# Optimization experiments

Hardware: AMD Instinct MI355X
Metric: run time of the kernel (lower is better)

Reference implementation:

```python
import jax, jax.numpy as jnp
import numpy as np

NUM_NODES = 25
EMBED_DIM = 64
OUT_SIZE = 2
N_TOTAL = 204800   # 8192 graphs * 25 nodes
N_EDGES = 3276800  # avg degree 16


def setup_inputs() -> dict:
    key = jax.random.key(0)
    ks = jax.random.split(key, 8)
    x = jax.random.normal(ks[0], (N_TOTAL, EMBED_DIM), dtype=jnp.float32)
    # random edges; real graphs are graph-local but math is identical
    edge_index = jax.random.randint(ks[1], (2, N_EDGES), 0, N_TOTAL, dtype=jnp.int32)
    batch = jnp.repeat(jnp.arange(N_TOTAL // NUM_NODES, dtype=jnp.int32), NUM_NODES)
    hid = NUM_NODES * EMBED_DIM  # 1600
    W_conv = jax.random.normal(ks[2], (EMBED_DIM, EMBED_DIM), dtype=jnp.float32) / np.sqrt(EMBED_DIM)
    b_conv = jnp.zeros((EMBED_DIM,), dtype=jnp.float32)
    W1 = jax.random.normal(ks[3], (hid, hid), dtype=jnp.float32) / np.sqrt(hid)
    b1 = jnp.zeros((hid,), dtype=jnp.float32)
    W2 = jax.random.normal(ks[4], (hid, OUT_SIZE), dtype=jnp.float32) / np.sqrt(hid)
    b2 = jnp.zeros((OUT_SIZE,), dtype=jnp.float32)
    return {"x": x, "edge_index": edge_index, "batch": batch,
            "W_conv": W_conv, "b_conv": b_conv,
            "W1": W1, "b1": b1, "W2": W2, "b2": b2}


def reference(x, edge_index, batch, W_conv, b_conv, W1, b1, W2, b2):
    N = x.shape[0]
    # --- GCNConv: add self-loops, symmetric degree norm, transform, scatter-add ---
    loop = jnp.arange(N, dtype=edge_index.dtype)
    src = jnp.concatenate([edge_index[0], loop])
    dst = jnp.concatenate([edge_index[1], loop])
    deg = jax.ops.segment_sum(jnp.ones_like(dst, dtype=x.dtype), dst, num_segments=N)
    dinv = jax.lax.rsqrt(deg)  # deg >= 1 due to self-loops
    norm = dinv[src] * dinv[dst]                       # [E+N]
    h = x @ W_conv                                     # [N, D]
    msg = h[src] * norm[:, None]                       # gather + scale
    h = jax.ops.segment_sum(msg, dst, num_segments=N) + b_conv
    h = jax.nn.relu(h)
    # --- dense head ---
    nb = -(-batch.shape[0] // NUM_NODES)               # ceil
    h = h.reshape(nb, NUM_NODES * EMBED_DIM)           # [B, 1600]
    h = jax.nn.relu(h @ W1 + b1)
    logits = h @ W2 + b2
    return jax.nn.softmax(logits, axis=-1)
```

## Files before the change

kernel.cpp:

```cpp
#include <hip/hip_runtime.h>
#include <hip/hip_bf16.h>
#include <stdint.h>

#define NT   204800
#define NE   3276800
#define ED   64
#define NBG  8192
#define HID  1600
#define HPAD 1664
#define CAP  56
#define NBKT 400
#define BCAP 9216

typedef float  f32x4  __attribute__((ext_vector_type(4)));
typedef __bf16 bf16x8 __attribute__((ext_vector_type(8)));

__device__ __forceinline__ void async_ld16(const void* g, void* l) {
    __builtin_amdgcn_global_load_lds(
        (__attribute__((address_space(1))) const void*)g,
        (__attribute__((address_space(3))) void*)l, 16, 0, 0);
}

__device__ __forceinline__ unsigned short f2bf_raw(float f) {
    __hip_bfloat16 h = __float2bfloat16(f);
    return *(unsigned short*)&h;
}

__global__ void k_initg(int* __restrict__ gcur) {
    int t = threadIdx.x;
    if (t < NBKT) gcur[t] = t * BCAP;
}

__global__ __launch_bounds__(256) void k_part(const int* __restrict__ srcv,
                                              const int* __restrict__ dstv,
                                              int* __restrict__ gcur,
                                              unsigned* __restrict__ rec) {
    __shared__ int hist[NBKT];
    __shared__ int slot[NBKT];
    __shared__ int gofs[NBKT];
    const int t = threadIdx.x;
    const int base = blockIdx.x * (NE / 512);
    for (int i = t; i < NBKT; i += 256) { hist[i] = 0; slot[i] = 0; }
    __syncthreads();
    for (int j = 0; j < 25; ++j) {
        int d = dstv[base + j * 256 + t];
        atomicAdd(&hist[d >> 9], 1);
    }
    __syncthreads();
    for (int i = t; i < NBKT; i += 256) gofs[i] = atomicAdd(&gcur[i], hist[i]);
    __syncthreads();
    for (int j = 0; j < 25; ++j) {
        int i = base + j * 256 + t;
        int d = dstv[i];
        int s = srcv[i];
        int b = d >> 9;
        int ls = atomicAdd(&slot[b], 1);
        int idx = gofs[b] + ls;
        if (idx < (b + 1) * BCAP)
            rec[idx] = ((unsigned)s << 9) | (unsigned)(d & 511);
    }
}

__global__ __launch_bounds__(512) void k_fillb(const int* __restrict__ gcur,
                                               const unsigned* __restrict__ rec,
                                               int* __restrict__ cur,
                                               int* __restrict__ csr,
                                               float* __restrict__ dinv) {
    __shared__ int cnt[512];
    const int t = threadIdx.x;
    const int b = blockIdx.x;
    const int n0 = b * 512;
    cnt[t] = 0;
    __syncthreads();
    const int bstart = b * BCAP;
    int bcnt = gcur[b] - bstart;
    bcnt = (bcnt > BCAP) ? BCAP : bcnt;
    for (int idx = t; idx < bcnt; idx += 512) {
        unsigned r = rec[bstart + idx];
        unsigned rel = r & 511u;
        int ls = atomicAdd(&cnt[rel], 1);
        if (ls < CAP) csr[(size_t)(n0 + rel) * CAP + ls] = (int)(r >> 9);
    }
    __syncthreads();
    int cn = cnt[t];
    cur[n0 + t] = cn;
    dinv[n0 + t] = rsqrtf((float)cn + 1.f);
}

__global__ __launch_bounds__(256) void k_gemm_conv(const float* __restrict__ x,
                                                   const float* __restrict__ Wc,
                                                   const float* __restrict__ dinv,
                                                   __hip_bfloat16* __restrict__ hbs) {
    __shared__ unsigned short Xs[64 * 72];
    __shared__ unsigned short Wt[64 * 72];
    const int t = threadIdx.x;
    const int row0 = blockIdx.x * 64;
#pragma unroll
    for (int i = 0; i < 4; ++i) {
        int idx = i * 256 + t;
        int r = idx >> 4, c4 = (idx & 15) << 2;
        f32x4 wv = ((const f32x4*)Wc)[idx];
        Wt[(c4 + 0) * 72 + r] = f2bf_raw(wv.x);
        Wt[(c4 + 1) * 72 + r] = f2bf_raw(wv.y);
        Wt[(c4 + 2) * 72 + r] = f2bf_raw(wv.z);
        Wt[(c4 + 3) * 72 + r] = f2bf_raw(wv.w);
        f32x4 xv = ((const f32x4*)(x + (size_t)row0 * 64))[idx];
        ushort4 p;
        p.x = f2bf_raw(xv.x);
        p.y = f2bf_raw(xv.y);
        p.z = f2bf_raw(xv.z);
        p.w = f2bf_raw(xv.w);
        *(ushort4*)&Xs[r * 72 + c4] = p;
    }
    __syncthreads();
    const int w = t >> 6, lane = t & 63;
    const int fr = lane & 15, fq = lane >> 4;
    f32x4 acc[4] = {};
#pragma unroll
    for (int kb = 0; kb < 2; ++kb) {
        bf16x8 av = *(const bf16x8*)&Xs[(w * 16 + fr) * 72 + kb * 32 + fq * 8];
#pragma unroll
        for (int j = 0; j < 4; ++j) {
            bf16x8 bv = *(const bf16x8*)&Wt[(j * 16 + fr) * 72 + kb * 32 + fq * 8];
            acc[j] = __builtin_amdgcn_mfma_f32_16x16x32_bf16(av, bv, acc[j], 0, 0, 0);
        }
    }
#pragma unroll
    for (int r = 0; r < 4; ++r) {
        int row = row0 + w * 16 + fq * 4 + r;
        float di = dinv[row];
        unsigned short* dst = (unsigned short*)&hbs[(size_t)row * 64];
#pragma unroll
        for (int j = 0; j < 4; ++j)
            dst[j * 16 + fr] = f2bf_raw(acc[j][r] * di);
    }
}

__global__ __launch_bounds__(256) void k_gather(const int* __restrict__ cur,
                                                const int* __restrict__ csr,
                                                const float* __restrict__ dinv,
                                                const __hip_bfloat16* __restrict__ hbs,
                                                const float* __restrict__ bc,
                                                __hip_bfloat16* __restrict__ Hb) {
    const int lane = threadIdx.x & 63;
    const int du = __builtin_amdgcn_readfirstlane(blockIdx.x * 4 + (threadIdx.x >> 6));
    const float di = dinv[du];
    int cn = cur[du];
    cn = (cn > CAP) ? CAP : cn;
    const int* __restrict__ lst = csr + (size_t)du * CAP;
    const float self = __bfloat162float(hbs[(size_t)du * ED + lane]);
    float acc = self;
    int e = 0;
    for (; e + 16 <= cn; e += 16) {
#pragma unroll
        for (int q = 0; q < 16; ++q) {
            int s = lst[e + q];
            acc += __bfloat162float(hbs[(size_t)s * ED + lane]);
        }
    }
    if (e < cn) {
        const int pad = e + 16 - cn;
#pragma unroll
        for (int q = 0; q < 16; ++q) {
            int s = (e + q < cn) ? lst[e + q] : du;
            acc += __bfloat162float(hbs[(size_t)s * ED + lane]);
        }
        acc = fmaf(-(float)pad, self, acc);
    }
    Hb[(size_t)du * ED + lane] = __float2bfloat16(fmaxf(bc[lane] + di * acc, 0.f));
}

__global__ void k_convW1(const float* __restrict__ W1, __hip_bfloat16* __restrict__ Bt) {
    __shared__ float tile[64][65];
    const int t = threadIdx.x;
    const int k0 = blockIdx.x * 64;
    const int n0 = blockIdx.y * 64;
#pragma unroll
    for (int i = 0; i < 16; ++i) {
        int lin = i * 256 + t;
        int r = lin >> 6, c = lin & 63;
        int n = n0 + c;
        tile[r][c] = (n < HID) ? W1[(size_t)(k0 + r) * HID + n] : 0.f;
    }
    __syncthreads();
#pragma unroll
    for (int i = 0; i < 16; ++i) {
        int lin = i * 256 + t;
        int nn = lin >> 6, kk = lin & 63;
        Bt[(size_t)(n0 + nn) * HID + k0 + kk] = __float2bfloat16(tile[kk][nn]);
    }
}

__global__ __launch_bounds__(256) void k_gemm1(const __hip_bfloat16* __restrict__ A,
                                               const __hip_bfloat16* __restrict__ Bt,
                                               const float* __restrict__ b1,
                                               __hip_bfloat16* __restrict__ h2) {
    __shared__ unsigned short As[128 * 32];
    __shared__ unsigned short Bs[128 * 32];
    const int t = threadIdx.x;
    const int lane = t & 63;
    const int wave = t >> 6;
    const int bm0 = blockIdx.x * 128;
    const int bn0 = blockIdx.y * 128;
    const int wm = (wave >> 1) * 64;
    const int wn = (wave & 1) * 64;
    const int fr = lane & 15;
    const int fq = lane >> 4;
    const int sr = t >> 2;
    const int sc = (t & 3) * 8;
    const __hip_bfloat16* ga0 = A + (size_t)(bm0 + sr) * HID + sc;
    const __hip_bfloat16* ga1 = A + (size_t)(bm0 + 64 + sr) * HID + sc;
    const __hip_bfloat16* gb0 = Bt + (size_t)(bn0 + sr) * HID + sc;
    const __hip_bfloat16* gb1 = Bt + (size_t)(bn0 + 64 + sr) * HID + sc;
    unsigned short* lA0 = &As[t * 8];
    unsigned short* lA1 = &As[(256 + t) * 8];
    unsigned short* lB0 = &Bs[t * 8];
    unsigned short* lB1 = &Bs[(256 + t) * 8];
    const unsigned short* fa0 = &As[(wm + fr) * 32 + fq * 8];
    const unsigned short* fb0 = &Bs[(wn + fr) * 32 + fq * 8];
    f32x4 acc[4][4] = {};
    for (int k0 = 0; k0 < HID; k0 += 32) {
        async_ld16(ga0, lA0); async_ld16(ga1, lA1);
        async_ld16(gb0, lB0); async_ld16(gb1, lB1);
        ga0 += 32; ga1 += 32; gb0 += 32; gb1 += 32;
        __syncthreads();
        bf16x8 av[4], bv[4];
#pragma unroll
        for (int i = 0; i < 4; ++i) av[i] = *(const bf16x8*)(fa0 + i * 16 * 32);
#pragma unroll
        for (int j = 0; j < 4; ++j) bv[j] = *(const bf16x8*)(fb0 + j * 16 * 32);
#pragma unroll
        for (int i = 0; i < 4; ++i)
#pragma unroll
            for (int j = 0; j < 4; ++j)
                acc[i][j] = __builtin_amdgcn_mfma_f32_16x16x32_bf16(av[i], bv[j], acc[i][j], 0, 0, 0);
        __syncthreads();
    }
#pragma unroll
    for (int j = 0; j < 4; ++j) {
        int n = bn0 + wn + j * 16 + fr;
        if (n < HID) {
            float bias = b1[n];
#pragma unroll
            for (int i = 0; i < 4; ++i) {
#pragma unroll
                for (int r = 0; r < 4; ++r) {
                    int m = bm0 + wm + i * 16 + fq * 4 + r;
                    float v = acc[i][j][r] + bias;
                    h2[(size_t)m * HID + n] = __float2bfloat16(fmaxf(v, 0.f));
                }
            }
        }
    }
}

__global__ void k_head(const __hip_bfloat16* __restrict__ h2, const float* __restrict__ W2,
                       const float* __restrict__ b2, float* __restrict__ out) {
    int g = blockIdx.x * 4 + (threadIdx.x >> 6);
    int lane = threadIdx.x & 63;
    const __hip_bfloat16* row = h2 + (size_t)g * HID;
    float a0 = 0.f, a1 = 0.f;
#pragma unroll
    for (int i = 0; i < 25; ++i) {
        int k = i * 64 + lane;
        float hv = __bfloat162float(row[k]);
        float2 w = ((const float2*)W2)[k];
        a0 += hv * w.x;
        a1 += hv * w.y;
    }
#pragma unroll
    for (int off = 32; off > 0; off >>= 1) {
        a0 += __shfl_down(a0, off, 64);
        a1 += __shfl_down(a1, off, 64);
    }
    if (lane == 0) {
        float l0 = a0 + b2[0], l1 = a1 + b2[1];
        float mx = fmaxf(l0, l1);
        float e0 = expf(l0 - mx), e1 = expf(l1 - mx);
        float s = e0 + e1;
        out[2 * g]     = e0 / s;
        out[2 * g + 1] = e1 / s;
    }
}

extern "C" void kernel_launch(void* const* d_in, const int* in_sizes, int n_in,
                              void* d_out, int out_size, void* d_ws, size_t ws_size,
                              hipStream_t stream) {
    const float* x  = (const float*)d_in[0];
    const int*   ei = (const int*)d_in[1];
    const float* Wc = (const float*)d_in[3];
    const float* bc = (const float*)d_in[4];
    const float* W1 = (const float*)d_in[5];
    const float* b1 = (const float*)d_in[6];
    const float* W2 = (const float*)d_in[7];
    const float* b2 = (const float*)d_in[8];
    float* out = (float*)d_out;

    const int* srcv = ei;
    const int* dstv = ei + NE;

    char* ws = (char*)d_ws;
    int*   cur  = (int*)ws;
    float* dinv = (float*)(ws + 819200);
    int*   gcur = (int*)(ws + 1638400);
    int*   csr  = (int*)(ws + 1642496);
    unsigned* rec = (unsigned*)(ws + 47517696);
    __hip_bfloat16* hbs = (__hip_bfloat16*)(ws + 47517696);
    __hip_bfloat16* h2  = (__hip_bfloat16*)(ws + 47517696);
    __hip_bfloat16* Hb  = (__hip_bfloat16*)(ws + 73732096);
    __hip_bfloat16* Bt  = (__hip_bfloat16*)(ws + 99946496);

    k_initg    <<<1, 512, 0, stream>>>(gcur);
    k_part     <<<512, 256, 0, stream>>>(srcv, dstv, gcur, rec);
    k_fillb    <<<NBKT, 512, 0, stream>>>(gcur, rec, cur, csr, dinv);
    k_gemm_conv<<<NT / 64, 256, 0, stream>>>(x, Wc, dinv, hbs);
    k_gather   <<<NT / 4, 256, 0, stream>>>(cur, csr, dinv, hbs, bc, Hb);
    k_convW1   <<<dim3(HID / 64, HPAD / 64), 256, 0, stream>>>(W1, Bt);
    k_gemm1    <<<dim3(NBG / 128, HPAD / 128), 256, 0, stream>>>(Hb, Bt, b1, h2);
    k_head     <<<NBG / 4, 256, 0, stream>>>(h2, W2, b2, out);
}
```

Measured before the change: 385.0 us.

## Cache bucket slots in partition, binary-tail gather, swizzle GEMM1 LDS, larger gather blocks

The partition kernel now records each edge's local slot from the first histogram pass in registers. This avoids rereading dst and doing a second round of shared atomics. The gather kernel replaces its padded 16-wide tail (which loaded the self row and subtracted it back out) with 8/4/2/1 remainder steps, and now runs 16 nodes per 1024-thread block. GEMM1 applies an XOR swizzle to the LDS column chunks so fragment reads avoid bank conflicts. Risks include register pressure from the 25-entry keep array and lower scheduling flexibility with the larger blocks.

```diff
diff --git a/kernel.cpp b/kernel.cpp
--- a/kernel.cpp
+++ b/kernel.cpp
@@ -36,28 +36,31 @@
                                               int* __restrict__ gcur,
                                               unsigned* __restrict__ rec) {
     __shared__ int hist[NBKT];
-    __shared__ int slot[NBKT];
     __shared__ int gofs[NBKT];
     const int t = threadIdx.x;
     const int base = blockIdx.x * (NE / 512);
-    for (int i = t; i < NBKT; i += 256) { hist[i] = 0; slot[i] = 0; }
-    __syncthreads();
+    for (int i = t; i < NBKT; i += 256) hist[i] = 0;
+    __syncthreads();
+    unsigned keep[25];
+#pragma unroll
     for (int j = 0; j < 25; ++j) {
         int d = dstv[base + j * 256 + t];
-        atomicAdd(&hist[d >> 9], 1);
+        int b = d >> 9;
+        int ls = atomicAdd(&hist[b], 1);
+        keep[j] = ((unsigned)ls << 18) | ((unsigned)(d & 511) << 9) | (unsigned)b;
     }
     __syncthreads();
     for (int i = t; i < NBKT; i += 256) gofs[i] = atomicAdd(&gcur[i], hist[i]);
     __syncthreads();
+#pragma unroll
     for (int j = 0; j < 25; ++j) {
-        int i = base + j * 256 + t;
-        int d = dstv[i];
-        int s = srcv[i];
-        int b = d >> 9;
-        int ls = atomicAdd(&slot[b], 1);
-        int idx = gofs[b] + ls;
+        int s = srcv[base + j * 256 + t];
+        unsigned k = keep[j];
+        int b   = (int)(k & 511u);
+        int rel = (int)((k >> 9) & 511u);
+        int idx = gofs[b] + (int)(k >> 18);
         if (idx < (b + 1) * BCAP)
-            rec[idx] = ((unsigned)s << 9) | (unsigned)(d & 511);
+            rec[idx] = ((unsigned)s << 9) | (unsigned)rel;
     }
 }
 
@@ -136,20 +139,19 @@
     }
 }
 
-__global__ __launch_bounds__(256) void k_gather(const int* __restrict__ cur,
-                                                const int* __restrict__ csr,
-                                                const float* __restrict__ dinv,
-                                                const __hip_bfloat16* __restrict__ hbs,
-                                                const float* __restrict__ bc,
-                                                __hip_bfloat16* __restrict__ Hb) {
+__global__ __launch_bounds__(1024) void k_gather(const int* __restrict__ cur,
+                                                 const int* __restrict__ csr,
+                                                 const float* __restrict__ dinv,
+                                                 const __hip_bfloat16* __restrict__ hbs,
+                                                 const float* __restrict__ bc,
+                                                 __hip_bfloat16* __restrict__ Hb) {
     const int lane = threadIdx.x & 63;
-    const int du = __builtin_amdgcn_readfirstlane(blockIdx.x * 4 + (threadIdx.x >> 6));
+    const int du = __builtin_amdgcn_readfirstlane(blockIdx.x * 16 + (threadIdx.x >> 6));
     const float di = dinv[du];
     int cn = cur[du];
     cn = (cn > CAP) ? CAP : cn;
     const int* __restrict__ lst = csr + (size_t)du * CAP;
-    const float self = __bfloat162float(hbs[(size_t)du * ED + lane]);
-    float acc = self;
+    float acc = __bfloat162float(hbs[(size_t)du * ED + lane]);
     int e = 0;
     for (; e + 16 <= cn; e += 16) {
 #pragma unroll
@@ -158,14 +160,33 @@
             acc += __bfloat162float(hbs[(size_t)s * ED + lane]);
         }
     }
-    if (e < cn) {
-        const int pad = e + 16 - cn;
-#pragma unroll
-        for (int q = 0; q < 16; ++q) {
-            int s = (e + q < cn) ? lst[e + q] : du;
+    if (cn & 8) {
+#pragma unroll
+        for (int q = 0; q < 8; ++q) {
+            int s = lst[e + q];
             acc += __bfloat162float(hbs[(size_t)s * ED + lane]);
         }
-        acc = fmaf(-(float)pad, self, acc);
+        e += 8;
+    }
+    if (cn & 4) {
+#pragma unroll
+        for (int q = 0; q < 4; ++q) {
+            int s = lst[e + q];
+            acc += __bfloat162float(hbs[(size_t)s * ED + lane]);
+        }
+        e += 4;
+    }
+    if (cn & 2) {
+#pragma unroll
+        for (int q = 0; q < 2; ++q) {
+            int s = lst[e + q];
+            acc += __bfloat162float(hbs[(size_t)s * ED + lane]);
+        }
+        e += 2;
+    }
+    if (cn & 1) {
+        int s = lst[e];
+        acc += __bfloat162float(hbs[(size_t)s * ED + lane]);
     }
     Hb[(size_t)du * ED + lane] = __float2bfloat16(fmaxf(bc[lane] + di * acc, 0.f));
 }
@@ -207,17 +228,18 @@
     const int fr = lane & 15;
     const int fq = lane >> 4;
     const int sr = t >> 2;
-    const int sc = (t & 3) * 8;
-    const __hip_bfloat16* ga0 = A + (size_t)(bm0 + sr) * HID + sc;
-    const __hip_bfloat16* ga1 = A + (size_t)(bm0 + 64 + sr) * HID + sc;
-    const __hip_bfloat16* gb0 = Bt + (size_t)(bn0 + sr) * HID + sc;
-    const __hip_bfloat16* gb1 = Bt + (size_t)(bn0 + 64 + sr) * HID + sc;
+    const int scs = (((t & 3) ^ ((sr >> 1) & 3)) * 8);
+    const __hip_bfloat16* ga0 = A + (size_t)(bm0 + sr) * HID + scs;
+    const __hip_bfloat16* ga1 = A + (size_t)(bm0 + 64 + sr) * HID + scs;
+    const __hip_bfloat16* gb0 = Bt + (size_t)(bn0 + sr) * HID + scs;
+    const __hip_bfloat16* gb1 = Bt + (size_t)(bn0 + 64 + sr) * HID + scs;
     unsigned short* lA0 = &As[t * 8];
     unsigned short* lA1 = &As[(256 + t) * 8];
     unsigned short* lB0 = &Bs[t * 8];
     unsigned short* lB1 = &Bs[(256 + t) * 8];
-    const unsigned short* fa0 = &As[(wm + fr) * 32 + fq * 8];
-    const unsigned short* fb0 = &Bs[(wn + fr) * 32 + fq * 8];
+    const int rdx = (fr >> 1) & 3;
+    const unsigned short* fa0 = &As[(wm + fr) * 32 + (fq ^ rdx) * 8];
+    const unsigned short* fb0 = &Bs[(wn + fr) * 32 + (fq ^ rdx) * 8];
     f32x4 acc[4][4] = {};
     for (int k0 = 0; k0 < HID; k0 += 32) {
         async_ld16(ga0, lA0); async_ld16(ga1, lA1);
@@ -314,7 +336,7 @@
     k_part     <<<512, 256, 0, stream>>>(srcv, dstv, gcur, rec);
     k_fillb    <<<NBKT, 512, 0, stream>>>(gcur, rec, cur, csr, dinv);
     k_gemm_conv<<<NT / 64, 256, 0, stream>>>(x, Wc, dinv, hbs);
-    k_gather   <<<NT / 4, 256, 0, stream>>>(cur, csr, dinv, hbs, bc, Hb);
+    k_gather   <<<NT / 16, 1024, 0, stream>>>(cur, csr, dinv, hbs, bc, Hb);
     k_convW1   <<<dim3(HID / 64, HPAD / 64), 256, 0, stream>>>(W1, Bt);
     k_gemm1    <<<dim3(NBG / 128, HPAD / 128), 256, 0, stream>>>(Hb, Bt, b1, h2);
     k_head     <<<NBG / 4, 256, 0, stream>>>(h2, W2, b2, out);
```

Result: slower. 394.3 us (+2.4%).
